# Optimization experiments

Measured on AMD Instinct MI355X. Metric: run time of the kernel, lower is better.

## Reference

```python
import jax, jax.numpy as jnp
import numpy as np

_LEVELS = jnp.array([-4, -2, -1, 0, 1, 2, 4], dtype=jnp.int32)  # shift-quant 7-value grid 'A'

B, S = 1, 512
IN_F, OUT_F = 4096, 16384
BLOCK = 64
NUM_BLOCKS = (IN_F + BLOCK - 1) // BLOCK  # 64


def setup_inputs() -> dict:
    key = jax.random.key(0)
    k1, k2, k3, k4 = jax.random.split(key, 4)
    x = jax.random.normal(k1, (B, S, IN_F), dtype=jnp.float32)
    idx = jax.random.randint(k2, (OUT_F, IN_F), 0, 7)
    q_weight = _LEVELS[idx]  # int32 values in {-4,-2,-1,0,1,2,4}
    scales = (jax.random.uniform(k3, (OUT_F, NUM_BLOCKS), dtype=jnp.float32) * 0.05 + 0.001).astype(jnp.float16)
    bias = (jax.random.normal(k4, (OUT_F,), dtype=jnp.float32) * 0.02).astype(jnp.float16)
    return {"x": x, "q_weight": q_weight, "scales": scales, "bias": bias, "block_size": BLOCK}


def reference(x, q_weight, scales, bias, block_size):
    # shift_matmul: dequantize blockwise-scaled power-of-two int8 weights, then GEMM.
    out_f, in_f = q_weight.shape
    # broadcast per-block fp16 scales along the in_features axis (handles padding block)
    w_scale = jnp.repeat(scales.astype(jnp.float32), block_size, axis=1)[:, :in_f]  # [out, in]
    w = q_weight.astype(jnp.float32) * w_scale  # [out, in]
    out = jnp.einsum("bsi,oi->bso", x, w)
    out = out + bias.astype(out.dtype)
    return out.astype(x.dtype)
```

## Files before the change

### kernel.cpp

```cpp
#include <hip/hip_runtime.h>
#include <hip/hip_bf16.h>
#include <stdint.h>


#define MM 512
#define NN 16384
#define KK 4096
#define BN 64
#define BK 128
#define NKB (KK / BK)

typedef __bf16 bf16x8 __attribute__((ext_vector_type(8)));
typedef float floatx4 __attribute__((ext_vector_type(4)));

__device__ __forceinline__ unsigned int pk_bf16_rtn(float lo, float hi) {
    __hip_bfloat162 h = __float22bfloat162_rn(float2{lo, hi});
    return *reinterpret_cast<unsigned int*>(&h);
}

__global__ __launch_bounds__(256) void pack_x(const float* __restrict__ x,
                                              unsigned short* __restrict__ xp) {
    const int t    = blockIdx.x * 256 + threadIdx.x;
    const int lane = t & 63;
    const int mt   = (t >> 6) & 31;
    const int ks   = (t >> 11) & 3;
    const int kb   = t >> 13;
    const int m    = mt * 16 + (lane & 15);
    const int k    = kb * 128 + ks * 32 + (lane >> 4) * 8;
    const float* px = x + (size_t)m * KK + k;
    const float4 a = *(const float4*)px;
    const float4 b = *(const float4*)(px + 4);
    uint4 o;
    o.x = pk_bf16_rtn(a.x, a.y);
    o.y = pk_bf16_rtn(a.z, a.w);
    o.z = pk_bf16_rtn(b.x, b.y);
    o.w = pk_bf16_rtn(b.z, b.w);
    *(uint4*)(xp + (size_t)t * 8) = o;
}

template <bool PRE>
__global__ __launch_bounds__(1024, 4) void qlin_gemm(
    const float* __restrict__ xf,
    const unsigned short* __restrict__ xp,
    const int* __restrict__ qw,
    const float* __restrict__ scales,
    const float* __restrict__ bias,
    float* __restrict__ out)
{
    __shared__ unsigned short sB[2][BN * BK];

    const int t    = threadIdx.x;
    const int lane = t & 63;
    const int w    = t >> 6;
    const int ln   = lane & 15;
    const int quad = lane >> 4;
    const int n0   = blockIdx.x * BN;

    const int r    = t >> 4;
    const int oct  = t & 15;
    const int ksp  = oct >> 2;
    const int jp   = r >> 4;
    const int ldst = (((oct & 3) << 4) + (r & 15)) ^ (ksp << 1);
    const int woff = ((ksp * 4 + jp) * 64 + ldst) * 8;
    const int* qp  = qw + (size_t)(n0 + r) * KK + oct * 8;
    const float* sp = scales + (size_t)(n0 + r) * 64 + (oct >> 3);

    floatx4 acc[2][4];
#pragma unroll
    for (int i = 0; i < 2; ++i)
#pragma unroll
        for (int j = 0; j < 4; ++j)
            acc[i][j] = (floatx4)0.0f;

    int4 qv0 = *(const int4*)(qp);
    int4 qv1 = *(const int4*)(qp + 4);
    float s  = sp[0];

    for (int kb = 0; kb < NKB; ++kb) {
        unsigned short* sb = sB[kb & 1];
        uint4 u;
        u.x = pk_bf16_rtn((float)qv0.x * s, (float)qv0.y * s);
        u.y = pk_bf16_rtn((float)qv0.z * s, (float)qv0.w * s);
        u.z = pk_bf16_rtn((float)qv1.x * s, (float)qv1.y * s);
        u.w = pk_bf16_rtn((float)qv1.z * s, (float)qv1.w * s);
        *(uint4*)(sb + woff) = u;

        if (kb + 1 < NKB) {
            qv0 = *(const int4*)(qp + (size_t)(kb + 1) * BK);
            qv1 = *(const int4*)(qp + (size_t)(kb + 1) * BK + 4);
            s   = sp[(size_t)(kb + 1) * 2];
        }

        __syncthreads();

        bf16x8 a[4][2];
        const unsigned short* xpb = xp + (size_t)kb * (4 * 32 * 64 * 8);
#pragma unroll
        for (int ks = 0; ks < 4; ++ks) {
            if constexpr (PRE) {
                const unsigned short* ap = xpb + (size_t)((ks * 32 + w * 2) * 64 + lane) * 8;
                a[ks][0] = *(const bf16x8*)(ap);
                a[ks][1] = *(const bf16x8*)(ap + 512);
            } else {
                const int k = kb * BK + ks * 32 + quad * 8;
#pragma unroll
                for (int i = 0; i < 2; ++i) {
                    const float* px = xf + (size_t)(w * 32 + i * 16 + ln) * KK + k;
                    const float4 f0 = *(const float4*)px;
                    const float4 f1 = *(const float4*)(px + 4);
                    uint4 ua;
                    ua.x = pk_bf16_rtn(f0.x, f0.y);
                    ua.y = pk_bf16_rtn(f0.z, f0.w);
                    ua.z = pk_bf16_rtn(f1.x, f1.y);
                    ua.w = pk_bf16_rtn(f1.z, f1.w);
                    a[ks][i] = *(bf16x8*)&ua;
                }
            }
        }
#pragma unroll
        for (int ks = 0; ks < 4; ++ks) {
            bf16x8 bfr[4];
#pragma unroll
            for (int j = 0; j < 4; ++j)
                bfr[j] = *(const bf16x8*)(sb + ((ks * 4 + j) * 64 + (lane ^ (ks << 1))) * 8);
#pragma unroll
            for (int j = 0; j < 4; ++j) {
                acc[0][j] = __builtin_amdgcn_mfma_f32_16x16x32_bf16(a[ks][0], bfr[j], acc[0][j], 0, 0, 0);
                acc[1][j] = __builtin_amdgcn_mfma_f32_16x16x32_bf16(a[ks][1], bfr[j], acc[1][j], 0, 0, 0);
            }
        }
    }

#pragma unroll
    for (int j = 0; j < 4; ++j) {
        const int n = n0 + j * 16 + ln;
        const float bv = bias[n];
#pragma unroll
        for (int i = 0; i < 2; ++i) {
            const int mbase = w * 32 + i * 16 + quad * 4;
#pragma unroll
            for (int rr = 0; rr < 4; ++rr)
                out[(size_t)(mbase + rr) * NN + n] = acc[i][j][rr] + bv;
        }
    }
}

extern "C" void kernel_launch(void* const* d_in, const int* in_sizes, int n_in,
                              void* d_out, int out_size, void* d_ws, size_t ws_size,
                              hipStream_t stream) {
    const float* x    = (const float*)d_in[0];
    const int* qw     = (const int*)d_in[1];
    const float* scl  = (const float*)d_in[2];
    const float* bias = (const float*)d_in[3];
    float* out        = (float*)d_out;

    dim3 grid(NN / BN);
    dim3 block(1024);

    if (ws_size >= (size_t)MM * KK * sizeof(unsigned short)) {
        unsigned short* xp = (unsigned short*)d_ws;
        pack_x<<<dim3(MM * KK / (256 * 8)), dim3(256), 0, stream>>>(x, xp);
        qlin_gemm<true><<<grid, block, 0, stream>>>(x, xp, qw, scl, bias, out);
    } else {
        qlin_gemm<false><<<grid, block, 0, stream>>>(x, nullptr, qw, scl, bias, out);
    }
}
```

Measured before the change: 421.6 us.

## Halve N tile to 32, use 512-thread blocks with 64-row warps, nontemporal weight loads

The N tile per block shrinks from 64 to 32 columns and the block from 1024 to 512 threads. Each warp now covers 64 M rows by 32 N columns (4x2 MFMA tiles) instead of 32x64, and the grid doubles to 512 blocks. Weight loads become nontemporal to avoid polluting cache with streamed int32 weights. __syncthreads is replaced by a barrier that waits only on LDS, issued before the next prefetch. The larger grid is meant to fill more CUs, at the cost of reading the packed activations twice as often per output column.

```diff
diff --git a/kernel.cpp b/kernel.cpp
--- a/kernel.cpp
+++ b/kernel.cpp
@@ -6,12 +6,17 @@
 #define MM 512
 #define NN 16384
 #define KK 4096
-#define BN 64
+#define BN 32
 #define BK 128
 #define NKB (KK / BK)
 
 typedef __bf16 bf16x8 __attribute__((ext_vector_type(8)));
 typedef float floatx4 __attribute__((ext_vector_type(4)));
+typedef int intx4 __attribute__((ext_vector_type(4)));
+
+__device__ __forceinline__ void barrier_nodrain() {
+    asm volatile("s_waitcnt lgkmcnt(0)\n\ts_barrier" ::: "memory");
+}
 
 __device__ __forceinline__ unsigned int pk_bf16_rtn(float lo, float hi) {
     __hip_bfloat162 h = __float22bfloat162_rn(float2{lo, hi});
@@ -39,7 +44,7 @@
 }
 
 template <bool PRE>
-__global__ __launch_bounds__(1024, 4) void qlin_gemm(
+__global__ __launch_bounds__(512, 4) void qlin_gemm(
     const float* __restrict__ xf,
     const unsigned short* __restrict__ xp,
     const int* __restrict__ qw,
@@ -60,24 +65,25 @@
     const int oct  = t & 15;
     const int ksp  = oct >> 2;
     const int jp   = r >> 4;
-    const int ldst = (((oct & 3) << 4) + (r & 15)) ^ (ksp << 1);
-    const int woff = ((ksp * 4 + jp) * 64 + ldst) * 8;
+    const int ldst = (((oct & 3) << 4) | (r & 15)) ^ (ksp << 1);
+    const int woff = ((ksp * 2 + jp) * 64 + ldst) * 8;
     const int* qp  = qw + (size_t)(n0 + r) * KK + oct * 8;
     const float* sp = scales + (size_t)(n0 + r) * 64 + (oct >> 3);
 
-    floatx4 acc[2][4];
+    floatx4 acc[4][2];
 #pragma unroll
-    for (int i = 0; i < 2; ++i)
+    for (int i = 0; i < 4; ++i)
 #pragma unroll
-        for (int j = 0; j < 4; ++j)
+        for (int j = 0; j < 2; ++j)
             acc[i][j] = (floatx4)0.0f;
 
-    int4 qv0 = *(const int4*)(qp);
-    int4 qv1 = *(const int4*)(qp + 4);
+    intx4 qv0 = __builtin_nontemporal_load((const intx4*)(qp));
+    intx4 qv1 = __builtin_nontemporal_load((const intx4*)(qp + 4));
     float s  = sp[0];
 
     for (int kb = 0; kb < NKB; ++kb) {
         unsigned short* sb = sB[kb & 1];
+
         uint4 u;
         u.x = pk_bf16_rtn((float)qv0.x * s, (float)qv0.y * s);
         u.y = pk_bf16_rtn((float)qv0.z * s, (float)qv0.w * s);
@@ -85,27 +91,27 @@
         u.w = pk_bf16_rtn((float)qv1.z * s, (float)qv1.w * s);
         *(uint4*)(sb + woff) = u;
 
+        barrier_nodrain();
+
         if (kb + 1 < NKB) {
-            qv0 = *(const int4*)(qp + (size_t)(kb + 1) * BK);
-            qv1 = *(const int4*)(qp + (size_t)(kb + 1) * BK + 4);
+            qv0 = __builtin_nontemporal_load((const intx4*)(qp + (size_t)(kb + 1) * BK));
+            qv1 = __builtin_nontemporal_load((const intx4*)(qp + (size_t)(kb + 1) * BK + 4));
             s   = sp[(size_t)(kb + 1) * 2];
         }
 
-        __syncthreads();
-
-        bf16x8 a[4][2];
         const unsigned short* xpb = xp + (size_t)kb * (4 * 32 * 64 * 8);
 #pragma unroll
         for (int ks = 0; ks < 4; ++ks) {
+            bf16x8 a[4];
             if constexpr (PRE) {
-                const unsigned short* ap = xpb + (size_t)((ks * 32 + w * 2) * 64 + lane) * 8;
-                a[ks][0] = *(const bf16x8*)(ap);
-                a[ks][1] = *(const bf16x8*)(ap + 512);
+#pragma unroll
+                for (int i = 0; i < 4; ++i)
+                    a[i] = *(const bf16x8*)(xpb + (size_t)((ks * 32 + w * 4 + i) * 64 + lane) * 8);
             } else {
                 const int k = kb * BK + ks * 32 + quad * 8;
 #pragma unroll
-                for (int i = 0; i < 2; ++i) {
-                    const float* px = xf + (size_t)(w * 32 + i * 16 + ln) * KK + k;
+                for (int i = 0; i < 4; ++i) {
+                    const float* px = xf + (size_t)(w * 64 + i * 16 + ln) * KK + k;
                     const float4 f0 = *(const float4*)px;
                     const float4 f1 = *(const float4*)(px + 4);
                     uint4 ua;
@@ -113,31 +119,28 @@
                     ua.y = pk_bf16_rtn(f0.z, f0.w);
                     ua.z = pk_bf16_rtn(f1.x, f1.y);
                     ua.w = pk_bf16_rtn(f1.z, f1.w);
-                    a[ks][i] = *(bf16x8*)&ua;
+                    a[i] = *(bf16x8*)&ua;
                 }
             }
-        }
+            bf16x8 bfr[2];
 #pragma unroll
-        for (int ks = 0; ks < 4; ++ks) {
-            bf16x8 bfr[4];
+            for (int j = 0; j < 2; ++j)
+                bfr[j] = *(const bf16x8*)(sb + ((ks * 2 + j) * 64 + (lane ^ (ks << 1))) * 8);
 #pragma unroll
-            for (int j = 0; j < 4; ++j)
-                bfr[j] = *(const bf16x8*)(sb + ((ks * 4 + j) * 64 + (lane ^ (ks << 1))) * 8);
+            for (int i = 0; i < 4; ++i)
 #pragma unroll
-            for (int j = 0; j < 4; ++j) {
-                acc[0][j] = __builtin_amdgcn_mfma_f32_16x16x32_bf16(a[ks][0], bfr[j], acc[0][j], 0, 0, 0);
-                acc[1][j] = __builtin_amdgcn_mfma_f32_16x16x32_bf16(a[ks][1], bfr[j], acc[1][j], 0, 0, 0);
-            }
+                for (int j = 0; j < 2; ++j)
+                    acc[i][j] = __builtin_amdgcn_mfma_f32_16x16x32_bf16(a[i], bfr[j], acc[i][j], 0, 0, 0);
         }
     }
 
 #pragma unroll
-    for (int j = 0; j < 4; ++j) {
+    for (int j = 0; j < 2; ++j) {
         const int n = n0 + j * 16 + ln;
         const float bv = bias[n];
 #pragma unroll
-        for (int i = 0; i < 2; ++i) {
-            const int mbase = w * 32 + i * 16 + quad * 4;
+        for (int i = 0; i < 4; ++i) {
+            const int mbase = w * 64 + i * 16 + quad * 4;
 #pragma unroll
             for (int rr = 0; rr < 4; ++rr)
                 out[(size_t)(mbase + rr) * NN + n] = acc[i][j][rr] + bv;
@@ -155,7 +158,7 @@
     float* out        = (float*)d_out;
 
     dim3 grid(NN / BN);
-    dim3 block(1024);
+    dim3 block(512);
 
     if (ws_size >= (size_t)MM * KK * sizeof(unsigned short)) {
         unsigned short* xp = (unsigned short*)d_ws;
```

Result: slower. 446.8 us (+6.0%).
